# Kernel optimization log

Measured on AMD Instinct MI355X. Metric: run time of the kernel, lower is better.

## Reference

```python
import jax, jax.numpy as jnp
import numpy as np

B, L = 1, 4096
VOCAB, D = 32000, 2048
NQ, NKV, HD = 16, 8, 128
EXPAND = NQ // NKV
SCALING = HD ** -0.5
SOFTCAP = 50.0
ROPE_THETA = 10000.0
RATIO = 0.25


def setup_inputs() -> dict:
    key = jax.random.key(0)
    k1, k2, k3, k4 = jax.random.split(key, 4)
    return {
        "input_ids": jax.random.randint(k1, (B, L), 0, VOCAB, dtype=jnp.int32),
        "embed_table": jax.random.normal(k2, (VOCAB, D), dtype=jnp.float32) * 0.02,
        "wq": jax.random.normal(k3, (D, NQ * HD), dtype=jnp.float32) * 0.02,
        "wk": jax.random.normal(k4, (D, NKV * HD), dtype=jnp.float32) * 0.02,
    }


def _rotate_half(x):
    h = x.shape[-1] // 2
    return jnp.concatenate([-x[..., h:], x[..., :h]], axis=-1)


def _importance(input_ids, embed_table, wq, wk):
    """QK + RoPE + softcap + causal softmax -> head/query-averaged importance [B, L]."""
    embs = embed_table[input_ids]  # [B, L, D]
    # rotary cos/sin: [1, 1, L, HD]
    inv_freq = 1.0 / (ROPE_THETA ** (jnp.arange(0, HD, 2, dtype=jnp.float32) / HD))
    freqs = jnp.arange(L, dtype=jnp.float32)[:, None] * inv_freq[None, :]  # [L, HD/2]
    emb = jnp.concatenate([freqs, freqs], axis=-1)
    cos = jnp.cos(emb)[None, None]
    sin = jnp.sin(emb)[None, None]
    q = (embs @ wq).reshape(B, L, NQ, HD).transpose(0, 2, 1, 3)   # [B, NQ, L, HD]
    k = (embs @ wk).reshape(B, L, NKV, HD).transpose(0, 2, 1, 3)  # [B, NKV, L, HD]
    q = q * cos + _rotate_half(q) * sin
    k = k * cos + _rotate_half(k) * sin
    k = jnp.repeat(k, EXPAND, axis=1)  # GQA expand -> [B, NQ, L, HD]
    scores = jnp.einsum('bhqd,bhkd->bhqk', q, k) * SCALING
    scores = jnp.tanh(scores / SOFTCAP) * SOFTCAP
    causal = jnp.triu(jnp.full((L, L), -jnp.inf, dtype=scores.dtype), 1)
    attn = jax.nn.softmax(scores + causal, axis=-1)  # [B, NQ, L, L]
    return attn.mean(axis=(1, 2))  # mean over heads then queries -> [B, L]


def reference(input_ids, embed_table, wq, wk):
    importance = _importance(input_ids, embed_table, wq, wk)
    k_sel = max(int(L * RATIO), 2)
    _, topk = jax.lax.top_k(importance, k_sel)
    topk = jnp.sort(topk, axis=-1)
    # Original torch code does `if need_append:` which requires B == 1.
    # Concrete (eager) branch; with random inputs this is almost always True.
    if bool(topk[0, -1] != L - 1):
        topk = jnp.concatenate([topk, jnp.full((B, 1), L - 1, dtype=topk.dtype)], axis=1)
    pruned_ids = jnp.take_along_axis(input_ids, topk, axis=1)
    return pruned_ids, topk
```

## Files before the change

### kernel.cpp

```cpp
#include <hip/hip_runtime.h>
#include <hip/hip_bf16.h>
#include <math.h>

#define L_SEQ   4096
#define D_MODEL 2048
#define NQ      16
#define NKV     8
#define HD      128
#define CSTR    3072
#define SCALING 0.08838834764831845f
#define LOG2E   1.4426950408889634f
#define K_SEL   1024
#define CHUNK   8
#define NCHUNK  288

typedef __attribute__((ext_vector_type(8))) short bf16x8;
typedef __attribute__((ext_vector_type(4))) float f32x4;

__device__ __forceinline__ unsigned short f2bf(float f) {
  union { float f; unsigned u; } v; v.f = f;
  unsigned r = v.u + 0x7fffu + ((v.u >> 16) & 1u);
  return (unsigned short)(r >> 16);
}
__device__ __forceinline__ unsigned pk2(float a, float b) {
  return (__float_as_uint(b) & 0xffff0000u) | (__float_as_uint(a) >> 16);
}
__device__ __forceinline__ float bf2f(unsigned short b) {
  union { unsigned u; float f; } v; v.u = ((unsigned)b) << 16;
  return v.f;
}

typedef __attribute__((address_space(3))) unsigned int lds_u32;
typedef const __attribute__((address_space(1))) unsigned int glob_u32;
__device__ __forceinline__ void gl2lds16(const unsigned short* g, unsigned short* l) {
  __builtin_amdgcn_global_load_lds((glob_u32*)g, (lds_u32*)l, 16, 0, 0);
}

__global__ __launch_bounds__(256) void prep_w(
    const float* __restrict__ wq, const float* __restrict__ wk,
    unsigned short* __restrict__ Wt) {
  __shared__ __align__(16) unsigned short T[64][80];
  const int tid = threadIdx.x;
  const int nt = blockIdx.x;
  const int kt = blockIdx.y;
  const float* src; int srcN, n0;
  if (nt < 32) { src = wq; srcN = 2048; n0 = nt * 64; }
  else         { src = wk; srcN = 1024; n0 = (nt - 32) * 64; }
  const int k0 = kt * 64;
#pragma unroll
  for (int p = 0; p < 4; ++p) {
    const int idx = p * 256 + tid;
    const int row = idx >> 4;
    const int c4 = (idx & 15) * 4;
    float4 v = *(const float4*)(src + (size_t)(k0 + row) * srcN + n0 + c4);
    T[c4 + 0][row] = f2bf(v.x); T[c4 + 1][row] = f2bf(v.y);
    T[c4 + 2][row] = f2bf(v.z); T[c4 + 3][row] = f2bf(v.w);
  }
  __syncthreads();
#pragma unroll
  for (int p = 0; p < 2; ++p) {
    const int c = p * 256 + tid;
    const int n = c >> 3, k8 = (c & 7) * 8;
    *(uint4*)(Wt + (size_t)(nt * 64 + n) * D_MODEL + k0 + k8) = *(const uint4*)(&T[n][k8]);
  }
}

__global__ __launch_bounds__(256) void gemm_qk(
    const int* __restrict__ ids, const float* __restrict__ table,
    const unsigned short* __restrict__ Wt, unsigned short* __restrict__ C) {
  __shared__ __align__(16) unsigned short As[128 * 32];
  __shared__ __align__(16) unsigned short Bs[128 * 32];
  const int tid = threadIdx.x;
  const int w = tid >> 6, lane = tid & 63;
  const int quad = lane >> 4, lr = lane & 15;
  const int m0 = blockIdx.y * 128, n0 = blockIdx.x * 128;
  const int wm = (w >> 1) * 64, wn = (w & 1) * 64;

  const int arow = tid >> 1, ahalf = tid & 1;
  const float* aptr = table + (size_t)ids[m0 + arow] * D_MODEL + ahalf * 16;
  unsigned short* asl = &As[arow * 32 + ahalf * 16];

  const unsigned short* bptr =
      Wt + (size_t)(n0 + w * 16 + (lane >> 2)) * D_MODEL + (lane & 3) * 8;
  unsigned short* bsl0 = &Bs[(w * 16) * 32];
  unsigned short* bsl1 = &Bs[(64 + w * 16) * 32];

  f32x4 acc[4][4];
#pragma unroll
  for (int i = 0; i < 4; ++i)
#pragma unroll
    for (int j = 0; j < 4; ++j) acc[i][j] = (f32x4){0.f, 0.f, 0.f, 0.f};

  for (int k0 = 0; k0 < D_MODEL; k0 += 32) {
    __syncthreads();
    gl2lds16(bptr + k0, bsl0);
    gl2lds16(bptr + 64 * D_MODEL + k0, bsl1);
    const float4 f0 = *(const float4*)(aptr + k0);
    const float4 f1 = *(const float4*)(aptr + k0 + 4);
    const float4 f2 = *(const float4*)(aptr + k0 + 8);
    const float4 f3 = *(const float4*)(aptr + k0 + 12);
    uint4 u0, u1;
    u0.x = pk2(f0.x, f0.y); u0.y = pk2(f0.z, f0.w);
    u0.z = pk2(f1.x, f1.y); u0.w = pk2(f1.z, f1.w);
    u1.x = pk2(f2.x, f2.y); u1.y = pk2(f2.z, f2.w);
    u1.z = pk2(f3.x, f3.y); u1.w = pk2(f3.z, f3.w);
    *(uint4*)(asl) = u0;
    *(uint4*)(asl + 8) = u1;
    __syncthreads();
    bf16x8 af[4], bfr[4];
#pragma unroll
    for (int mt = 0; mt < 4; ++mt)
      af[mt] = *(const bf16x8*)&As[(wm + mt * 16 + lr) * 32 + quad * 8];
#pragma unroll
    for (int nt = 0; nt < 4; ++nt)
      bfr[nt] = *(const bf16x8*)&Bs[(wn + nt * 16 + lr) * 32 + quad * 8];
#pragma unroll
    for (int mt = 0; mt < 4; ++mt)
#pragma unroll
      for (int nt = 0; nt < 4; ++nt)
        acc[mt][nt] = __builtin_amdgcn_mfma_f32_16x16x32_bf16(af[mt], bfr[nt], acc[mt][nt], 0, 0, 0);
  }
#pragma unroll
  for (int mt = 0; mt < 4; ++mt) {
    const int row = m0 + wm + mt * 16 + quad * 4;
#pragma unroll
    for (int nt = 0; nt < 4; ++nt) {
      const int col = n0 + wn + nt * 16 + lr;
#pragma unroll
      for (int r = 0; r < 4; ++r)
        C[(size_t)(row + r) * CSTR + col] = f2bf(acc[mt][nt][r]);
    }
  }
}

__global__ void rope_all(unsigned short* __restrict__ C) {
  const int g = blockIdx.x * blockDim.x + threadIdx.x;
  const int t = g & 63;
  const int hi = g >> 6;
  const int h = hi % 24;
  const int i = hi / 24;
  const float e = (float)(2 * t) / 128.0f;
  const float invf = 1.0f / powf(10000.0f, e);
  const float ang = (float)i * invf;
  const float c = cosf(ang), s = sinf(ang);
  const size_t base = (size_t)i * CSTR + h * HD + t;
  const float x1 = bf2f(C[base]), x2 = bf2f(C[base + 64]);
  C[base]      = f2bf(x1 * c - x2 * s);
  C[base + 64] = f2bf(x2 * c + x1 * s);
}

__device__ __forceinline__ void chunk_map(int bidx, int& bx, int& ch) {
  int rem = bidx;
  for (int b = 63; b >= 0; --b) {
    const int nc = (b + 2 + CHUNK - 1) >> 3;
    if (rem < nc) { bx = b; ch = rem; return; }
    rem -= nc;
  }
  bx = 0; ch = 0;
}

__device__ __forceinline__ void stage_k(
    const unsigned short* __restrict__ kb_lane,
    unsigned short* buf, int j0, int w) {
#pragma unroll
  for (int p = 0; p < 4; ++p)
    gl2lds16(kb_lane + (size_t)(j0 + p * 16) * CSTR, &buf[(p * 16 + w * 4) * 128]);
}

__global__ __launch_bounds__(256) void attn_z(
    const unsigned short* __restrict__ Qb,
    const unsigned short* __restrict__ Kb,
    float* __restrict__ Z) {
  __shared__ __align__(16) unsigned short Ks[2][64 * 128];
  const int tid = threadIdx.x;
  const int w = tid >> 6, lane = tid & 63;
  const int quad = lane >> 4, lr = lane & 15;
  const int kvh = blockIdx.y;
  int bx, ch; chunk_map(blockIdx.x, bx, ch);
  const int q0 = bx * 64;
  const int t0 = ch * CHUNK;
  const int t1 = min(t0 + CHUNK, bx + 1);

  const int srow = w * 4 + (lane >> 4);
  const int scol = (lane & 15) ^ (srow & 7);
  const unsigned short* kb_lane = Kb + (size_t)srow * CSTR + kvh * HD + scol * 8;

  int coff[4];
#pragma unroll
  for (int m = 0; m < 4; ++m) coff[m] = (((m * 4 + quad) ^ (lr & 7)) * 8);

  bf16x8 aq[2][4];
  const size_t rowb = (size_t)(q0 + w * 16 + lr) * CSTR;
#pragma unroll
  for (int hh = 0; hh < 2; ++hh)
#pragma unroll
    for (int m = 0; m < 4; ++m)
      aq[hh][m] = *(const bf16x8*)(Qb + rowb + (2 * kvh + hh) * HD + m * 32 + quad * 8);

  float zp[2][4] = {};

  stage_k(kb_lane, Ks[0], t0 * 64, w);
  __syncthreads();
  int cur = 0;
  for (int t = t0; t < t1; ++t) {
    if (t + 1 < t1) stage_k(kb_lane, Ks[cur ^ 1], (t + 1) * 64, w);
    const unsigned short* kbuf = Ks[cur];
    const bool diag = (t == bx);
    const int nsub = diag ? (w + 1) : 4;
    for (int sub = 0; sub < nsub; ++sub) {
      bf16x8 bfr[4];
#pragma unroll
      for (int m = 0; m < 4; ++m)
        bfr[m] = *(const bf16x8*)&kbuf[(sub * 16 + lr) * 128 + coff[m]];
      const bool masked = diag && (sub == w);
#pragma unroll
      for (int hh = 0; hh < 2; ++hh) {
        f32x4 acc = {0.f, 0.f, 0.f, 0.f};
#pragma unroll
        for (int m = 0; m < 4; ++m)
          acc = __builtin_amdgcn_mfma_f32_16x16x32_bf16(aq[hh][m], bfr[m], acc, 0, 0, 0);
#pragma unroll
        for (int r = 0; r < 4; ++r) {
          float e = exp2f(acc[r] * (SCALING * LOG2E));
          if (masked && lr > quad * 4 + r) e = 0.0f;
          zp[hh][r] += e;
        }
      }
    }
    __syncthreads();
    cur ^= 1;
  }
#pragma unroll
  for (int hh = 0; hh < 2; ++hh)
#pragma unroll
    for (int r = 0; r < 4; ++r) {
      float z = zp[hh][r];
      z += __shfl_xor(z, 1); z += __shfl_xor(z, 2);
      z += __shfl_xor(z, 4); z += __shfl_xor(z, 8);
      if (lr == 0)
        atomicAdd(&Z[(size_t)(2 * kvh + hh) * L_SEQ + q0 + w * 16 + quad * 4 + r], z);
    }
}

__global__ __launch_bounds__(256) void attn_col(
    const unsigned short* __restrict__ Qb,
    const unsigned short* __restrict__ Kb,
    const float* __restrict__ Z, float* __restrict__ imp) {
  __shared__ __align__(16) unsigned short Ks[2][64 * 128];
  const int tid = threadIdx.x;
  const int w = tid >> 6, lane = tid & 63;
  const int quad = lane >> 4, lr = lane & 15;
  const int kvh = blockIdx.y;
  int bx, ch; chunk_map(blockIdx.x, bx, ch);
  const int q0 = bx * 64;
  const int t0 = ch * CHUNK;
  const int t1 = min(t0 + CHUNK, bx + 1);

  const int srow = w * 4 + (lane >> 4);
  const int scol = (lane & 15) ^ (srow & 7);
  const unsigned short* kb_lane = Kb + (size_t)srow * CSTR + kvh * HD + scol * 8;

  int coff[4];
#pragma unroll
  for (int m = 0; m < 4; ++m) coff[m] = (((m * 4 + quad) ^ (lr & 7)) * 8);

  bf16x8 aq[2][4];
  const size_t rowb = (size_t)(q0 + w * 16 + lr) * CSTR;
#pragma unroll
  for (int hh = 0; hh < 2; ++hh)
#pragma unroll
    for (int m = 0; m < 4; ++m)
      aq[hh][m] = *(const bf16x8*)(Qb + rowb + (2 * kvh + hh) * HD + m * 32 + quad * 8);

  float l2r[2][4];
#pragma unroll
  for (int hh = 0; hh < 2; ++hh)
#pragma unroll
    for (int r = 0; r < 4; ++r)
      l2r[hh][r] = -__log2f(Z[(size_t)(2 * kvh + hh) * L_SEQ + q0 + w * 16 + quad * 4 + r]);

  stage_k(kb_lane, Ks[0], t0 * 64, w);
  __syncthreads();
  int cur = 0;
  for (int t = t0; t < t1; ++t) {
    if (t + 1 < t1) stage_k(kb_lane, Ks[cur ^ 1], (t + 1) * 64, w);
    __builtin_amdgcn_sched_barrier(0);
    const unsigned short* kbuf = Ks[cur];
    const bool diag = (t == bx);
    const int nsub = diag ? (w + 1) : 4;
    for (int sub = 0; sub < nsub; ++sub) {
      bf16x8 bfr[4];
#pragma unroll
      for (int m = 0; m < 4; ++m)
        bfr[m] = *(const bf16x8*)&kbuf[(sub * 16 + lr) * 128 + coff[m]];
      const bool masked = diag && (sub == w);
      float csum = 0.0f;
#pragma unroll
      for (int hh = 0; hh < 2; ++hh) {
        f32x4 acc = {0.f, 0.f, 0.f, 0.f};
#pragma unroll
        for (int m = 0; m < 4; ++m)
          acc = __builtin_amdgcn_mfma_f32_16x16x32_bf16(aq[hh][m], bfr[m], acc, 0, 0, 0);
#pragma unroll
        for (int r = 0; r < 4; ++r) {
          float e = exp2f(__builtin_fmaf(acc[r], SCALING * LOG2E, l2r[hh][r]));
          if (masked && lr > quad * 4 + r) e = 0.0f;
          csum += e;
        }
      }
      csum += __shfl_xor(csum, 16);
      csum += __shfl_xor(csum, 32);
      if (lane < 16) atomicAdd(&imp[t * 64 + sub * 16 + lr], csum);
    }
    asm volatile("s_waitcnt vmcnt(4) lgkmcnt(0)" ::: "memory");
    __builtin_amdgcn_s_barrier();
    cur ^= 1;
  }
}

__global__ __launch_bounds__(1024) void topk_kernel(
    const float* __restrict__ imp, const int* __restrict__ ids,
    int* __restrict__ out, int out_size) {
  __shared__ float v[L_SEQ];
  __shared__ int ix[L_SEQ];
  __shared__ int sel[K_SEL + 1];
  const int tid = threadIdx.x;
  for (int i = tid; i < L_SEQ; i += 1024) { v[i] = imp[i]; ix[i] = i; }
  __syncthreads();
  for (int k = 2; k <= L_SEQ; k <<= 1) {
    for (int j = k >> 1; j > 0; j >>= 1) {
#pragma unroll 1
      for (int t = tid; t < L_SEQ / 2; t += 1024) {
        const int i = ((t & ~(j - 1)) << 1) | (t & (j - 1));
        const int l = i | j;
        const float vi = v[i], vl = v[l];
        const bool desc = ((i & k) == 0);
        if (desc ? (vi < vl) : (vi > vl)) {
          v[i] = vl; v[l] = vi;
          const int tmp = ix[i]; ix[i] = ix[l]; ix[l] = tmp;
        }
      }
      __syncthreads();
    }
  }
  sel[tid] = ix[tid];
  __syncthreads();
  for (int k = 2; k <= K_SEL; k <<= 1) {
    for (int j = k >> 1; j > 0; j >>= 1) {
      if (tid < K_SEL / 2) {
        const int i = ((tid & ~(j - 1)) << 1) | (tid & (j - 1));
        const int l = i | j;
        const int si = sel[i], sl = sel[l];
        const bool asc = ((i & k) == 0);
        if (asc ? (si > sl) : (si < sl)) { sel[i] = sl; sel[l] = si; }
      }
      __syncthreads();
    }
  }
  if (tid == 0) sel[K_SEL] = L_SEQ - 1;
  __syncthreads();
  const int half = out_size >> 1;
  for (int i = tid; i < half; i += 1024) {
    const int idx2 = (i < K_SEL) ? sel[i] : sel[K_SEL];
    out[half + i] = idx2;
    out[i] = ids[idx2];
  }
}

extern "C" void kernel_launch(void* const* d_in, const int* in_sizes, int n_in,
                              void* d_out, int out_size, void* d_ws, size_t ws_size,
                              hipStream_t stream) {
  const int*   ids   = (const int*)d_in[0];
  const float* table = (const float*)d_in[1];
  const float* wq    = (const float*)d_in[2];
  const float* wk    = (const float*)d_in[3];
  char* ws = (char*)d_ws;
  unsigned short* Wt = (unsigned short*)ws;
  unsigned short* C  = (unsigned short*)(ws + 12ull * 1024 * 1024);
  float* imp = (float*)(ws + 36ull * 1024 * 1024);
  float* Z   = (float*)(ws + 36ull * 1024 * 1024 + 16384);
  int* out = (int*)d_out;

  hipMemsetAsync(imp, 0, L_SEQ * sizeof(float), stream);
  hipMemsetAsync(Z, 0, NQ * L_SEQ * sizeof(float), stream);

  dim3 blk(256);
  prep_w<<<dim3(48, 32), blk, 0, stream>>>(wq, wk, Wt);
  gemm_qk<<<dim3(CSTR / 128, L_SEQ / 128), blk, 0, stream>>>(ids, table, Wt, C);
  rope_all<<<(L_SEQ * 24 * 64) / 256, blk, 0, stream>>>(C);
  attn_z<<<dim3(NCHUNK, NKV), blk, 0, stream>>>(C, C + 2048, Z);
  attn_col<<<dim3(NCHUNK, NKV), blk, 0, stream>>>(C, C + 2048, Z, imp);
  topk_kernel<<<1, 1024, 0, stream>>>(imp, ids, out, out_size);
}
```

Measured before the change: 652.2 us.

## Use radix-select top-k, LDS column accumulation, and precomputed RoPE table

Replaces the full bitonic sort over 4096 scores plus the index re-sort with a 4-pass 8-bit radix select and a prefix-scan compaction, which emits the selected indices already in ascending order. RoPE cos/sin are precomputed once into a table, and the rope pass is vectorised to four elements per thread. attn_col accumulates per-block column sums in LDS before doing global atomics, and loads Z as float4. It also replaces the custom waitcnt barrier with __syncthreads and drops the sched barrier, which may reduce copy/compute overlap.

```diff
diff --git a/kernel.cpp b/kernel.cpp
--- a/kernel.cpp
+++ b/kernel.cpp
@@ -133,20 +133,38 @@
   }
 }
 
-__global__ void rope_all(unsigned short* __restrict__ C) {
+__global__ __launch_bounds__(256) void rope_tab(float2* __restrict__ tab) {
   const int g = blockIdx.x * blockDim.x + threadIdx.x;
   const int t = g & 63;
-  const int hi = g >> 6;
+  const int i = g >> 6;
+  const float invf = exp2f((float)t * (-13.287712379549449f / 64.0f));
+  const float ang = (float)i * invf;
+  tab[g] = make_float2(cosf(ang), sinf(ang));
+}
+
+__global__ __launch_bounds__(256) void rope_all(
+    unsigned short* __restrict__ C, const float2* __restrict__ tab) {
+  const int g = blockIdx.x * blockDim.x + threadIdx.x;
+  const int t4 = (g & 15) * 4;
+  const int hi = g >> 4;
   const int h = hi % 24;
   const int i = hi / 24;
-  const float e = (float)(2 * t) / 128.0f;
-  const float invf = 1.0f / powf(10000.0f, e);
-  const float ang = (float)i * invf;
-  const float c = cosf(ang), s = sinf(ang);
-  const size_t base = (size_t)i * CSTR + h * HD + t;
-  const float x1 = bf2f(C[base]), x2 = bf2f(C[base + 64]);
-  C[base]      = f2bf(x1 * c - x2 * s);
-  C[base + 64] = f2bf(x2 * c + x1 * s);
+  const size_t base = (size_t)i * CSTR + h * HD + t4;
+  ushort4 a = *(const ushort4*)(C + base);
+  ushort4 b = *(const ushort4*)(C + base + 64);
+  const float2 cs0 = tab[i * 64 + t4 + 0];
+  const float2 cs1 = tab[i * 64 + t4 + 1];
+  const float2 cs2 = tab[i * 64 + t4 + 2];
+  const float2 cs3 = tab[i * 64 + t4 + 3];
+  const float a0 = bf2f(a.x), a1 = bf2f(a.y), a2 = bf2f(a.z), a3 = bf2f(a.w);
+  const float b0 = bf2f(b.x), b1 = bf2f(b.y), b2 = bf2f(b.z), b3 = bf2f(b.w);
+  ushort4 ra, rb;
+  ra.x = f2bf(a0 * cs0.x - b0 * cs0.y); rb.x = f2bf(b0 * cs0.x + a0 * cs0.y);
+  ra.y = f2bf(a1 * cs1.x - b1 * cs1.y); rb.y = f2bf(b1 * cs1.x + a1 * cs1.y);
+  ra.z = f2bf(a2 * cs2.x - b2 * cs2.y); rb.z = f2bf(b2 * cs2.x + a2 * cs2.y);
+  ra.w = f2bf(a3 * cs3.x - b3 * cs3.y); rb.w = f2bf(b3 * cs3.x + a3 * cs3.y);
+  *(ushort4*)(C + base) = ra;
+  *(ushort4*)(C + base + 64) = rb;
 }
 
 __device__ __forceinline__ void chunk_map(int bidx, int& bx, int& ch) {
@@ -247,6 +265,7 @@
     const unsigned short* __restrict__ Kb,
     const float* __restrict__ Z, float* __restrict__ imp) {
   __shared__ __align__(16) unsigned short Ks[2][64 * 128];
+  __shared__ float colacc[CHUNK * 64];
   const int tid = threadIdx.x;
   const int w = tid >> 6, lane = tid & 63;
   const int quad = lane >> 4, lr = lane & 15;
@@ -274,17 +293,18 @@
 
   float l2r[2][4];
 #pragma unroll
-  for (int hh = 0; hh < 2; ++hh)
-#pragma unroll
-    for (int r = 0; r < 4; ++r)
-      l2r[hh][r] = -__log2f(Z[(size_t)(2 * kvh + hh) * L_SEQ + q0 + w * 16 + quad * 4 + r]);
+  for (int hh = 0; hh < 2; ++hh) {
+    const float4 z4 = *(const float4*)&Z[(size_t)(2 * kvh + hh) * L_SEQ + q0 + w * 16 + quad * 4];
+    l2r[hh][0] = -__log2f(z4.x); l2r[hh][1] = -__log2f(z4.y);
+    l2r[hh][2] = -__log2f(z4.z); l2r[hh][3] = -__log2f(z4.w);
+  }
 
   stage_k(kb_lane, Ks[0], t0 * 64, w);
+  for (int c = tid; c < CHUNK * 64; c += 256) colacc[c] = 0.0f;
   __syncthreads();
   int cur = 0;
   for (int t = t0; t < t1; ++t) {
     if (t + 1 < t1) stage_k(kb_lane, Ks[cur ^ 1], (t + 1) * 64, w);
-    __builtin_amdgcn_sched_barrier(0);
     const unsigned short* kbuf = Ks[cur];
     const bool diag = (t == bx);
     const int nsub = diag ? (w + 1) : 4;
@@ -310,55 +330,103 @@
       }
       csum += __shfl_xor(csum, 16);
       csum += __shfl_xor(csum, 32);
-      if (lane < 16) atomicAdd(&imp[t * 64 + sub * 16 + lr], csum);
-    }
-    asm volatile("s_waitcnt vmcnt(4) lgkmcnt(0)" ::: "memory");
-    __builtin_amdgcn_s_barrier();
+      if (lane < 16) atomicAdd(&colacc[(t - t0) * 64 + sub * 16 + lr], csum);
+    }
+    __syncthreads();
     cur ^= 1;
   }
+  const int ncol = (t1 - t0) * 64;
+  const int jb = t0 * 64;
+  for (int c = tid; c < ncol; c += 256) atomicAdd(&imp[jb + c], colacc[c]);
 }
 
 __global__ __launch_bounds__(1024) void topk_kernel(
     const float* __restrict__ imp, const int* __restrict__ ids,
     int* __restrict__ out, int out_size) {
-  __shared__ float v[L_SEQ];
-  __shared__ int ix[L_SEQ];
+  __shared__ unsigned vals[L_SEQ];
+  __shared__ unsigned hist[256];
+  __shared__ unsigned bc[2];
+  __shared__ int wsum[16];
+  __shared__ int wsum2[16];
   __shared__ int sel[K_SEL + 1];
   const int tid = threadIdx.x;
-  for (int i = tid; i < L_SEQ; i += 1024) { v[i] = imp[i]; ix[i] = i; }
-  __syncthreads();
-  for (int k = 2; k <= L_SEQ; k <<= 1) {
-    for (int j = k >> 1; j > 0; j >>= 1) {
+  const int lane = tid & 63, wv = tid >> 6;
+
+  for (int i = tid; i < L_SEQ; i += 1024) vals[i] = __float_as_uint(imp[i]);
+  __syncthreads();
+
+  unsigned prefix = 0;
+  int remaining = K_SEL;
 #pragma unroll 1
-      for (int t = tid; t < L_SEQ / 2; t += 1024) {
-        const int i = ((t & ~(j - 1)) << 1) | (t & (j - 1));
-        const int l = i | j;
-        const float vi = v[i], vl = v[l];
-        const bool desc = ((i & k) == 0);
-        if (desc ? (vi < vl) : (vi > vl)) {
-          v[i] = vl; v[l] = vi;
-          const int tmp = ix[i]; ix[i] = ix[l]; ix[l] = tmp;
-        }
+  for (int shift = 24; shift >= 0; shift -= 8) {
+    if (tid < 256) hist[tid] = 0;
+    __syncthreads();
+    const unsigned hmask = (shift == 24) ? 0u : (0xFFFFFFFFu << (shift + 8));
+    for (int i = tid; i < L_SEQ; i += 1024) {
+      const unsigned v = vals[i];
+      if ((v & hmask) == prefix) atomicAdd(&hist[(v >> shift) & 255u], 1u);
+    }
+    __syncthreads();
+    if (tid == 0) {
+      unsigned cum = 0;
+      for (int b = 255; b >= 0; --b) {
+        const unsigned h = hist[b];
+        if (cum + h >= (unsigned)remaining) { bc[0] = (unsigned)b; bc[1] = cum; break; }
+        cum += h;
       }
-      __syncthreads();
-    }
-  }
-  sel[tid] = ix[tid];
-  __syncthreads();
-  for (int k = 2; k <= K_SEL; k <<= 1) {
-    for (int j = k >> 1; j > 0; j >>= 1) {
-      if (tid < K_SEL / 2) {
-        const int i = ((tid & ~(j - 1)) << 1) | (tid & (j - 1));
-        const int l = i | j;
-        const int si = sel[i], sl = sel[l];
-        const bool asc = ((i & k) == 0);
-        if (asc ? (si > sl) : (si < sl)) { sel[i] = sl; sel[l] = si; }
-      }
-      __syncthreads();
-    }
-  }
+    }
+    __syncthreads();
+    prefix |= bc[0] << shift;
+    remaining -= (int)bc[1];
+    __syncthreads();
+  }
+  const unsigned T = prefix;
+
+  const int i0 = tid * 4;
+  const unsigned v0 = vals[i0], v1 = vals[i0 + 1], v2 = vals[i0 + 2], v3 = vals[i0 + 3];
+  const int e0 = (v0 == T), e1 = (v1 == T), e2 = (v2 == T), e3 = (v3 == T);
+  const int eqc = e0 + e1 + e2 + e3;
+
+  int x = eqc;
+#pragma unroll
+  for (int d = 1; d < 64; d <<= 1) { const int y = __shfl_up(x, d); if (lane >= d) x += y; }
+  if (lane == 63) wsum[wv] = x;
+  __syncthreads();
+  if (tid < 16) {
+    int s = wsum[tid];
+#pragma unroll
+    for (int d = 1; d < 16; d <<= 1) { const int y = __shfl_up(s, d); if (tid >= d) s += y; }
+    wsum[tid] = s;
+  }
+  __syncthreads();
+  const int eq_excl = (wv ? wsum[wv - 1] : 0) + x - eqc;
+  const int r0 = eq_excl, r1 = r0 + e0, r2 = r1 + e1, r3 = r2 + e2;
+  const int s0 = (v0 > T) || (e0 && r0 < remaining);
+  const int s1 = (v1 > T) || (e1 && r1 < remaining);
+  const int s2 = (v2 > T) || (e2 && r2 < remaining);
+  const int s3 = (v3 > T) || (e3 && r3 < remaining);
+  const int selc = s0 + s1 + s2 + s3;
+
+  int x2 = selc;
+#pragma unroll
+  for (int d = 1; d < 64; d <<= 1) { const int y = __shfl_up(x2, d); if (lane >= d) x2 += y; }
+  if (lane == 63) wsum2[wv] = x2;
+  __syncthreads();
+  if (tid < 16) {
+    int s = wsum2[tid];
+#pragma unroll
+    for (int d = 1; d < 16; d <<= 1) { const int y = __shfl_up(s, d); if (tid >= d) s += y; }
+    wsum2[tid] = s;
+  }
+  __syncthreads();
+  int pos = (wv ? wsum2[wv - 1] : 0) + x2 - selc;
+  if (s0) sel[pos++] = i0;
+  if (s1) sel[pos++] = i0 + 1;
+  if (s2) sel[pos++] = i0 + 2;
+  if (s3) sel[pos++] = i0 + 3;
   if (tid == 0) sel[K_SEL] = L_SEQ - 1;
   __syncthreads();
+
   const int half = out_size >> 1;
   for (int i = tid; i < half; i += 1024) {
     const int idx2 = (i < K_SEL) ? sel[i] : sel[K_SEL];
@@ -379,15 +447,17 @@
   unsigned short* C  = (unsigned short*)(ws + 12ull * 1024 * 1024);
   float* imp = (float*)(ws + 36ull * 1024 * 1024);
   float* Z   = (float*)(ws + 36ull * 1024 * 1024 + 16384);
+  float2* tab = (float2*)(ws + 36ull * 1024 * 1024 + 16384 + 262144);
   int* out = (int*)d_out;
 
   hipMemsetAsync(imp, 0, L_SEQ * sizeof(float), stream);
   hipMemsetAsync(Z, 0, NQ * L_SEQ * sizeof(float), stream);
 
   dim3 blk(256);
+  rope_tab<<<(L_SEQ * 64) / 256, blk, 0, stream>>>(tab);
   prep_w<<<dim3(48, 32), blk, 0, stream>>>(wq, wk, Wt);
   gemm_qk<<<dim3(CSTR / 128, L_SEQ / 128), blk, 0, stream>>>(ids, table, Wt, C);
-  rope_all<<<(L_SEQ * 24 * 64) / 256, blk, 0, stream>>>(C);
+  rope_all<<<(L_SEQ * 24 * 16) / 256, blk, 0, stream>>>(C, tab);
   attn_z<<<dim3(NCHUNK, NKV), blk, 0, stream>>>(C, C + 2048, Z);
   attn_col<<<dim3(NCHUNK, NKV), blk, 0, stream>>>(C, C + 2048, Z, imp);
   topk_kernel<<<1, 1024, 0, stream>>>(imp, ids, out, out_size);
```

New measurement: 621.9 us. -4.6%, faster.
